# Optimization experiments

Hardware: AMD Instinct MI355X
Metric: run time of the kernel (lower is better)

## Reference

```python
import jax, jax.numpy as jnp
import numpy as np

DIM = 1024
H = 16
DQK = 64   # head_qk_dim = dim*expand_k / num_heads
DV = 64    # head_v_dim
DIN = 4    # dim_inner (fast-weight rows)
CHUNK = 16
BASE_LR = 1e-3
KS = 4     # short conv kernel size
LN_EPS = 1e-5


def short_conv(x, w):
    """Causal depthwise conv1d (kernel KS) + identity residual.
    x: [b, l, c], w: [c, KS] (tap j multiplies x[t - (KS-1) + j])."""
    b, l, c = x.shape
    xp = jnp.pad(x, ((0, 0), (KS - 1, 0), (0, 0)))
    y = x  # residual: y = conv(x) + x
    for j in range(KS):
        y = y + xp[:, j:j + l, :] * w[None, None, :, j]
    return y


def setup_inputs() -> dict:
    key = jax.random.key(0)
    ks = jax.random.split(key, 16)
    b, l = 4, 2048
    key_dim, value_dim = H * DQK, H * DV
    inp = {
        "hidden_states": jax.random.normal(ks[0], (b, l, DIM), jnp.float32),
        "Wq": jax.random.normal(ks[1], (key_dim, DIM), jnp.float32) / np.sqrt(DIM),
        "Wk": jax.random.normal(ks[2], (key_dim, DIM), jnp.float32) / np.sqrt(DIM),
        "Wv": jax.random.normal(ks[3], (value_dim, DIM), jnp.float32) / np.sqrt(DIM),
        "Wlr": jax.random.normal(ks[4], (2 * H, DIM), jnp.float32) / np.sqrt(DIM),
        "Wo": jax.random.normal(ks[5], (DIM, value_dim), jnp.float32) / np.sqrt(value_dim),
        "Wg": jax.random.normal(ks[6], (DIM, value_dim), jnp.float32) / np.sqrt(value_dim),
        "conv_q": jax.random.normal(ks[7], (key_dim, KS), jnp.float32) / np.sqrt(KS),
        "conv_k": jax.random.normal(ks[8], (key_dim, KS), jnp.float32) / np.sqrt(KS),
        "conv_v": jax.random.normal(ks[9], (value_dim, KS), jnp.float32) / np.sqrt(KS),
        "W_in_init": jax.random.normal(ks[10], (1, DIN, H, DQK), jnp.float32) / np.sqrt(DQK),
        "W_out_init": jax.random.normal(ks[11], (1, DIN, H, DV), jnp.float32) / np.sqrt(DIN),
        "ln_gamma": jnp.ones((DV,), jnp.float32),
        "ln_beta": jnp.zeros((DV,), jnp.float32),
    }
    return inp


def reference(hidden_states, Wq, Wk, Wv, Wlr, Wo, Wg,
              conv_q, conv_k, conv_v, W_in_init, W_out_init, ln_gamma, ln_beta):
    b, l, _ = hidden_states.shape
    scale = 1.0 / np.sqrt(DQK)

    q = short_conv(hidden_states @ Wq.T, conv_q).reshape(b, l, H, DQK)
    k = short_conv(hidden_states @ Wk.T, conv_k).reshape(b, l, H, DQK)
    v = short_conv(hidden_states @ Wv.T, conv_v).reshape(b, l, H, DV)

    lr = jax.nn.softplus(hidden_states @ Wlr.T + BASE_LR).reshape(b, l, H, 2)

    nC = l // CHUNK
    # [nC, b, CHUNK, H, d] for scan over chunks
    qc = q.reshape(b, nC, CHUNK, H, DQK).transpose(1, 0, 2, 3, 4)
    kc = k.reshape(b, nC, CHUNK, H, DQK).transpose(1, 0, 2, 3, 4)
    vc = v.reshape(b, nC, CHUNK, H, DV).transpose(1, 0, 2, 3, 4)
    lrc = lr.reshape(b, nC, CHUNK, H, 2).transpose(1, 0, 2, 3, 4)

    W_in0 = jnp.broadcast_to(W_in_init, (b, DIN, H, DQK))
    W_out0 = jnp.broadcast_to(W_out_init, (b, DIN, H, DV))

    # causal mask: query t (abs pos DIN+t) sees keys j <= DIN+t
    mask = jnp.arange(DIN + CHUNK)[None, :] <= (jnp.arange(CHUNK)[:, None] + DIN)

    def step(carry, xs):
        W_in, W_out = carry
        qch, kch, vch, lrch = xs  # [b, CHUNK, H, d]
        Kf = jnp.concatenate([W_in, kch], axis=1)   # [b, DIN+CHUNK, H, DQK]
        Vf = jnp.concatenate([W_out, vch], axis=1)  # [b, DIN+CHUNK, H, DV]
        s = jnp.einsum('bthd,bshd->bhts', qch, Kf) * scale
        s = jnp.where(mask[None, None], s, -jnp.inf)
        o = jnp.einsum('bhts,bshd->bthd', jax.nn.softmax(s, axis=-1), Vf)

        # fast_kk update rule (non-causal attention, queries = W_in rows)
        g1 = jnp.einsum('bnhd,bchd->bhnc', W_in, kch) * scale
        Grad_out = -jnp.einsum('bhnc,bchd->bnhd', jax.nn.softmax(g1, -1), vch)
        g2 = jnp.einsum('bnhd,bchd->bhnc', W_in, kch * 0.5) * scale
        Grad_in = -jnp.einsum('bhnc,bchd->bnhd', jax.nn.softmax(g2, -1), kch)

        lr_mean = jnp.mean(lrch, axis=1, keepdims=True)  # [b,1,H,2]
        W_in_new = W_in - lr_mean[..., 0:1] * Grad_in
        W_out_new = W_out - lr_mean[..., 1:2] * Grad_out
        return (W_in_new, W_out_new), o

    _, os = jax.lax.scan(step, (W_in0, W_out0), (qc, kc, vc, lrc))
    o = os.transpose(1, 0, 2, 3, 4).reshape(b, l, H, DV)

    # LayerNorm over head_v_dim
    mu = o.mean(-1, keepdims=True)
    var = o.var(-1, keepdims=True)
    o = (o - mu) / jnp.sqrt(var + LN_EPS) * ln_gamma + ln_beta
    o = o.reshape(b, l, H * DV)

    gate = hidden_states @ Wg.T
    return (o * gate) @ Wo.T
```

## Files before the change

kernel.cpp:

```cpp
#include <hip/hip_runtime.h>
#include <hip/hip_bf16.h>
#include <math.h>

#define BATCH 4
#define SEQ   2048
#define DIM   1024
#define NH    16
#define DQK   64
#define DV    64
#define DIN   4
#define CHUNK 16
#define NC    128
#define KS    4
#define TOK   (BATCH*SEQ)
#define SCALE 0.125f
#define BASE_LR 1e-3f
#define LN_EPS 1e-5f
#define K3    3072

typedef float f32x4 __attribute__((ext_vector_type(4)));
typedef short s16x8 __attribute__((ext_vector_type(8)));

__device__ __forceinline__ unsigned short f2bf(float f) {
    unsigned u = __float_as_uint(f);
    u += 0x7fffu + ((u >> 16) & 1u);
    return (unsigned short)(u >> 16);
}
__device__ __forceinline__ float bf2f(unsigned short h) {
    return __uint_as_float(((unsigned)h) << 16);
}

__device__ __forceinline__ void gload_lds16(const void* g, void* l) {
    __builtin_amdgcn_global_load_lds(
        (const __attribute__((address_space(1))) void*)g,
        (__attribute__((address_space(3))) void*)l, 16, 0, 0);
}

__global__ __launch_bounds__(256) void split_bf16_kernel(
    const float* __restrict__ X, unsigned short* __restrict__ Y,
    int rows, int wmode)
{
    const int idx = blockIdx.x * 256 + threadIdx.x;
    if (idx >= rows * (DIM / 4)) return;
    const int r  = idx >> 8;
    const int c4 = (idx & 255) << 2;

    float4 x = *(const float4*)(X + (size_t)r * DIM + c4);
    ushort4 hv, lv;
    hv.x = f2bf(x.x); lv.x = f2bf(x.x - bf2f(hv.x));
    hv.y = f2bf(x.y); lv.y = f2bf(x.y - bf2f(hv.y));
    hv.z = f2bf(x.z); lv.z = f2bf(x.z - bf2f(hv.z));
    hv.w = f2bf(x.w); lv.w = f2bf(x.w - bf2f(hv.w));

    const size_t rb = (size_t)r * K3;
    *(ushort4*)(Y + rb + c4)        = hv;
    *(ushort4*)(Y + rb + 1024 + c4) = wmode ? lv : hv;
    *(ushort4*)(Y + rb + 2048 + c4) = wmode ? hv : lv;
}

__global__ __launch_bounds__(256) void gemm_mfma_qkvg(
    const unsigned short* __restrict__ A, const unsigned short* __restrict__ B,
    float* __restrict__ Cq, float* __restrict__ Ck,
    float* __restrict__ Cv, float* __restrict__ Cg)
{
    __shared__ __align__(16) unsigned short sA[128 * 64];
    __shared__ __align__(16) unsigned short sB[128 * 64];

    const int tid  = threadIdx.x;
    const int lane = tid & 63;
    const int wav  = tid >> 6;

    const int nbx = gridDim.x;
    const int nwg = nbx * gridDim.y;
    int flat = blockIdx.x + blockIdx.y * nbx;
    const int per = nwg >> 3;
    flat = (flat & 7) * per + (flat >> 3);
    const int m0 = (flat / nbx) * 128;
    const int n0 = (flat % nbx) * 128;

    const int wm = (wav >> 1) * 64;
    const int wn = (wav & 1) * 64;

    f32x4 acc[4][4] = {};

    const int fbase = wav * 64 + lane;
    const int lrow  = lane & 15;
    const int g     = lane >> 4;

    for (int kt = 0; kt < K3; kt += 64) {
        __syncthreads();
#pragma unroll
        for (int i = 0; i < 4; ++i) {
            const int f  = fbase + i * 256;
            const int r  = f >> 3;
            const int c  = (f & 7) ^ (r & 7);
            const size_t go = (size_t)r * K3 + kt + c * 8;
            char* lb = (char*)sA + (wav * 64 + i * 256) * 16;
            gload_lds16(A + (size_t)m0 * K3 + go, lb);
        }
#pragma unroll
        for (int i = 0; i < 4; ++i) {
            const int f  = fbase + i * 256;
            const int r  = f >> 3;
            const int c  = (f & 7) ^ (r & 7);
            const size_t go = (size_t)r * K3 + kt + c * 8;
            char* lb = (char*)sB + (wav * 64 + i * 256) * 16;
            gload_lds16(B + (size_t)n0 * K3 + go, lb);
        }
        __syncthreads();

#pragma unroll
        for (int ks = 0; ks < 2; ++ks) {
            const int cbase = ks * 4 + g;
            s16x8 af[4], bfr[4];
#pragma unroll
            for (int mi = 0; mi < 4; ++mi) {
                const int r  = wm + mi * 16 + lrow;
                const int cs = cbase ^ (r & 7);
                af[mi] = *(const s16x8*)((const char*)sA + r * 128 + cs * 16);
            }
#pragma unroll
            for (int ni = 0; ni < 4; ++ni) {
                const int r  = wn + ni * 16 + lrow;
                const int cs = cbase ^ (r & 7);
                bfr[ni] = *(const s16x8*)((const char*)sB + r * 128 + cs * 16);
            }
#pragma unroll
            for (int mi = 0; mi < 4; ++mi)
#pragma unroll
                for (int ni = 0; ni < 4; ++ni)
                    acc[mi][ni] = __builtin_amdgcn_mfma_f32_16x16x32_bf16(
                        af[mi], bfr[ni], acc[mi][ni], 0, 0, 0);
        }
    }

    const int nblk = n0 >> 10;
    float* __restrict__ Co = (nblk == 0) ? Cq : (nblk == 1) ? Ck
                           : (nblk == 2) ? Cv : Cg;
    const int nc0 = (n0 & 1023) + wn;
    const int lcol = lane & 15;
    const int lq   = lane >> 4;
#pragma unroll
    for (int mi = 0; mi < 4; ++mi)
#pragma unroll
        for (int ni = 0; ni < 4; ++ni)
#pragma unroll
            for (int r = 0; r < 4; ++r) {
                const int m = m0 + wm + mi * 16 + lq * 4 + r;
                const int n = nc0 + ni * 16 + lcol;
                Co[(size_t)m * DIM + n] = acc[mi][ni][r];
            }
}

__global__ __launch_bounds__(256) void gemm_mfma_bt(
    const unsigned short* __restrict__ A, const unsigned short* __restrict__ B,
    float* __restrict__ C, int M, int N)
{
    __shared__ __align__(16) unsigned short sA[128 * 64];
    __shared__ __align__(16) unsigned short sB[128 * 64];

    const int tid  = threadIdx.x;
    const int lane = tid & 63;
    const int wav  = tid >> 6;

    const int nbx = gridDim.x;
    const int nwg = nbx * gridDim.y;
    int flat = blockIdx.x + blockIdx.y * nbx;
    const int per = nwg >> 3;
    flat = (flat & 7) * per + (flat >> 3);
    const int m0 = (flat / nbx) * 128;
    const int n0 = (flat % nbx) * 128;

    const int wm = (wav >> 1) * 64;
    const int wn = (wav & 1) * 64;

    f32x4 acc[4][4] = {};

    const int fbase = wav * 64 + lane;
    const int lrow  = lane & 15;
    const int g     = lane >> 4;

    for (int kt = 0; kt < K3; kt += 64) {
        __syncthreads();
#pragma unroll
        for (int i = 0; i < 4; ++i) {
            const int f  = fbase + i * 256;
            const int r  = f >> 3;
            const int c  = (f & 7) ^ (r & 7);
            const size_t go = (size_t)r * K3 + kt + c * 8;
            char* lb = (char*)sA + (wav * 64 + i * 256) * 16;
            gload_lds16(A + (size_t)m0 * K3 + go, lb);
        }
#pragma unroll
        for (int i = 0; i < 4; ++i) {
            const int f  = fbase + i * 256;
            const int r  = f >> 3;
            const int c  = (f & 7) ^ (r & 7);
            const size_t go = (size_t)r * K3 + kt + c * 8;
            char* lb = (char*)sB + (wav * 64 + i * 256) * 16;
            gload_lds16(B + (size_t)n0 * K3 + go, lb);
        }
        __syncthreads();

#pragma unroll
        for (int ks = 0; ks < 2; ++ks) {
            const int cbase = ks * 4 + g;
            s16x8 af[4], bfr[4];
#pragma unroll
            for (int mi = 0; mi < 4; ++mi) {
                const int r  = wm + mi * 16 + lrow;
                const int cs = cbase ^ (r & 7);
                af[mi] = *(const s16x8*)((const char*)sA + r * 128 + cs * 16);
            }
#pragma unroll
            for (int ni = 0; ni < 4; ++ni) {
                const int r  = wn + ni * 16 + lrow;
                const int cs = cbase ^ (r & 7);
                bfr[ni] = *(const s16x8*)((const char*)sB + r * 128 + cs * 16);
            }
#pragma unroll
            for (int mi = 0; mi < 4; ++mi)
#pragma unroll
                for (int ni = 0; ni < 4; ++ni)
                    acc[mi][ni] = __builtin_amdgcn_mfma_f32_16x16x32_bf16(
                        af[mi], bfr[ni], acc[mi][ni], 0, 0, 0);
        }
    }

    const int lcol = lane & 15;
    const int lq   = lane >> 4;
#pragma unroll
    for (int mi = 0; mi < 4; ++mi)
#pragma unroll
        for (int ni = 0; ni < 4; ++ni)
#pragma unroll
            for (int r = 0; r < 4; ++r) {
                const int m = m0 + wm + mi * 16 + lq * 4 + r;
                const int n = n0 + wn + ni * 16 + lcol;
                C[(size_t)m * N + n] = acc[mi][ni][r];
            }
}

#define GBM 128
#define GBN 128
#define GBK 8

__global__ __launch_bounds__(256) void gemm_nt_f32(
    const float* __restrict__ A, const float* __restrict__ B,
    float* __restrict__ C, int M, int N, int K)
{
    __shared__ float As[GBK][GBM + 4];
    __shared__ float Bs[GBK][GBN + 4];

    const int tid = threadIdx.x;
    const int m0 = blockIdx.y * GBM;
    const int n0 = blockIdx.x * GBN;
    const int la_m = tid >> 1;
    const int la_k = (tid & 1) << 2;
    const int tm = tid >> 4;
    const int tn = tid & 15;

    float acc[8][8] = {};

    const float* Arow = A + (size_t)(m0 + la_m) * K + la_k;
    const float* Brow = B + (size_t)(n0 + la_m) * K + la_k;
    const bool bvalid = (n0 + la_m) < N;

    for (int k0 = 0; k0 < K; k0 += GBK) {
        float4 av = *(const float4*)(Arow + k0);
        float4 bv = make_float4(0.f, 0.f, 0.f, 0.f);
        if (bvalid) bv = *(const float4*)(Brow + k0);

        __syncthreads();
        As[la_k + 0][la_m] = av.x; As[la_k + 1][la_m] = av.y;
        As[la_k + 2][la_m] = av.z; As[la_k + 3][la_m] = av.w;
        Bs[la_k + 0][la_m] = bv.x; Bs[la_k + 1][la_m] = bv.y;
        Bs[la_k + 2][la_m] = bv.z; Bs[la_k + 3][la_m] = bv.w;
        __syncthreads();

#pragma unroll
        for (int k = 0; k < GBK; ++k) {
            float4 a0 = *(const float4*)&As[k][tm * 8];
            float4 a1 = *(const float4*)&As[k][tm * 8 + 4];
            float4 b0 = *(const float4*)&Bs[k][tn * 8];
            float4 b1 = *(const float4*)&Bs[k][tn * 8 + 4];
            float a[8] = {a0.x, a0.y, a0.z, a0.w, a1.x, a1.y, a1.z, a1.w};
            float b[8] = {b0.x, b0.y, b0.z, b0.w, b1.x, b1.y, b1.z, b1.w};
#pragma unroll
            for (int i = 0; i < 8; ++i)
#pragma unroll
                for (int j = 0; j < 8; ++j)
                    acc[i][j] += a[i] * b[j];
        }
    }

#pragma unroll
    for (int i = 0; i < 8; ++i) {
        const int m = m0 + tm * 8 + i;
#pragma unroll
        for (int j = 0; j < 8; ++j) {
            const int n = n0 + tn * 8 + j;
            if (n < N) C[(size_t)m * N + n] = acc[i][j];
        }
    }
}

__global__ __launch_bounds__(256) void conv_res_kernel(
    const float* __restrict__ x, const float* __restrict__ w,
    float* __restrict__ y)
{
    const int tid = blockIdx.x * blockDim.x + threadIdx.x;
    if (tid >= TOK * 256) return;
    const int c4  = (tid & 255) << 2;
    const int row = tid >> 8;
    const int t   = row & (SEQ - 1);

    const float* xp = x + (size_t)row * DIM + c4;
    float4 acc = *(const float4*)xp;
    float4 w0 = *(const float4*)(w + (c4 + 0) * 4);
    float4 w1 = *(const float4*)(w + (c4 + 1) * 4);
    float4 w2 = *(const float4*)(w + (c4 + 2) * 4);
    float4 w3 = *(const float4*)(w + (c4 + 3) * 4);

#pragma unroll
    for (int j = 0; j < 4; ++j) {
        const int tt = t - 3 + j;
        if (tt >= 0) {
            float4 xv = *(const float4*)(xp + (j - 3) * DIM);
            acc.x += xv.x * ((&w0.x)[j]);
            acc.y += xv.y * ((&w1.x)[j]);
            acc.z += xv.z * ((&w2.x)[j]);
            acc.w += xv.w * ((&w3.x)[j]);
        }
    }
    *(float4*)(y + (size_t)row * DIM + c4) = acc;
}

__global__ __launch_bounds__(256) void lrmean_kernel(
    const float* __restrict__ lrpre, float* __restrict__ lrm)
{
    const int idx = blockIdx.x * blockDim.x + threadIdx.x;
    if (idx >= BATCH * NC * NH * 2) return;
    const int j = idx & 1;
    const int h = (idx >> 1) & 15;
    const int c = (idx >> 5) & 127;
    const int b = idx >> 12;

    float s = 0.f;
#pragma unroll
    for (int i = 0; i < CHUNK; ++i) {
        float x = lrpre[((size_t)b * SEQ + c * CHUNK + i) * 32 + h * 2 + j] + BASE_LR;
        s += fmaxf(x, 0.f) + log1pf(expf(-fabsf(x)));
    }
    lrm[idx] = s * (1.f / CHUNK);
}

__global__ __launch_bounds__(64) void state_scan_kernel(
    const float* __restrict__ kconv, const float* __restrict__ vconv,
    const float* __restrict__ lrm,
    const float* __restrict__ win_init, const float* __restrict__ wout_init,
    float* __restrict__ wst_in, float* __restrict__ wst_out)
{
    const int bh = blockIdx.x;
    const int b = bh >> 4, h = bh & 15;
    const int d = threadIdx.x;

    __shared__ __align__(16) float sW[DIN][68];
    __shared__ __align__(16) float sK[CHUNK][68];
    __shared__ __align__(16) float sP1[DIN][16];
    __shared__ __align__(16) float sP2[DIN][16];
    __shared__ float sLR[NC * 2];

    float win[DIN], wout[DIN];
#pragma unroll
    for (int n = 0; n < DIN; ++n) {
        win[n]  = win_init [(n * NH + h) * DQK + d];
        wout[n] = wout_init[(n * NH + h) * DV  + d];
    }
#pragma unroll
    for (int i = 0; i < 4; ++i) {
        const int idx = d * 4 + i;
        const int c = idx >> 1, j = idx & 1;
        sLR[idx] = lrm[(((size_t)b * NC + c) * NH + h) * 2 + j];
    }

    const int gn = d >> 4;
    const int gc = d & 15;

    float ka[CHUNK], va[CHUNK], kb[CHUNK], vb[CHUNK];

    const size_t base00 = (size_t)b * SEQ * DIM + h * 64 + d;
#pragma unroll
    for (int i = 0; i < CHUNK; ++i) {
        ka[i] = kconv[base00 + (size_t)i * DIM];
        va[i] = vconv[base00 + (size_t)i * DIM];
    }
    asm volatile("s_waitcnt lgkmcnt(0)" ::: "memory");

#define SCAN_STEP(c, KC, VC, KN, VN)                                           \
    {                                                                          \
        if ((c) + 1 < NC) {                                                    \
            const size_t basen = base00 + (size_t)(((c) + 1) * CHUNK) * DIM;   \
            _Pragma("unroll")                                                  \
            for (int i = 0; i < CHUNK; ++i) {                                  \
                KN[i] = kconv[basen + (size_t)i * DIM];                        \
                VN[i] = vconv[basen + (size_t)i * DIM];                        \
            }                                                                  \
        }                                                                      \
        const size_t wofs = (((size_t)bh * NC + (c)) * DIN) * 64 + d;          \
        _Pragma("unroll")                                                      \
        for (int n = 0; n < DIN; ++n) {                                        \
            wst_in [wofs + n * 64] = win[n];                                   \
            wst_out[wofs + n * 64] = wout[n];                                  \
        }                                                                      \
        _Pragma("unroll")                                                      \
        for (int i = 0; i < CHUNK; ++i) sK[i][d] = KC[i];                      \
        _Pragma("unroll")                                                      \
        for (int n = 0; n < DIN; ++n) sW[n][d] = win[n];                       \
        asm volatile("s_waitcnt lgkmcnt(0)" ::: "memory");                     \
        float dot = 0.f;                                                       \
        _Pragma("unroll")                                                      \
        for (int q = 0; q < 16; ++q) {                                         \
            float4 wv = *(const float4*)&sW[gn][q * 4];                        \
            float4 xv = *(const float4*)&sK[gc][q * 4];                        \
            dot += wv.x * xv.x; dot += wv.y * xv.y;                            \
            dot += wv.z * xv.z; dot += wv.w * xv.w;                            \
        }                                                                      \
        float g1 = dot * SCALE;                                                \
        float g2 = dot * (0.5f * SCALE);                                       \
        float m1 = g1, m2 = g2;                                                \
        _Pragma("unroll")                                                      \
        for (int mk = 8; mk >= 1; mk >>= 1) {                                  \
            m1 = fmaxf(m1, __shfl_xor(m1, mk, 16));                            \
            m2 = fmaxf(m2, __shfl_xor(m2, mk, 16));                            \
        }                                                                      \
        float e1 = expf(g1 - m1), e2 = expf(g2 - m2);                          \
        float s1 = e1, s2 = e2;                                                \
        _Pragma("unroll")                                                      \
        for (int mk = 8; mk >= 1; mk >>= 1) {                                  \
            s1 += __shfl_xor(s1, mk, 16);                                      \
            s2 += __shfl_xor(s2, mk, 16);                                      \
        }                                                                      \
        sP1[gn][gc] = e1 / s1;                                                 \
        sP2[gn][gc] = e2 / s2;                                                 \
        asm volatile("s_waitcnt lgkmcnt(0)" ::: "memory");                     \
        const float lr0 = sLR[(c) * 2 + 0];                                    \
        const float lr1 = sLR[(c) * 2 + 1];                                    \
        _Pragma("unroll")                                                      \
        for (int n = 0; n < DIN; ++n) {                                        \
            float aI = 0.f, aO = 0.f;                                          \
            _Pragma("unroll")                                                  \
            for (int q = 0; q < 4; ++q) {                                      \
                float4 p2 = *(const float4*)&sP2[n][q * 4];                    \
                float4 p1 = *(const float4*)&sP1[n][q * 4];                    \
                aI += p2.x * KC[q * 4 + 0]; aI += p2.y * KC[q * 4 + 1];        \
                aI += p2.z * KC[q * 4 + 2]; aI += p2.w * KC[q * 4 + 3];        \
                aO += p1.x * VC[q * 4 + 0]; aO += p1.y * VC[q * 4 + 1];        \
                aO += p1.z * VC[q * 4 + 2]; aO += p1.w * VC[q * 4 + 3];        \
            }                                                                  \
            win[n]  += lr0 * aI;                                               \
            wout[n] += lr1 * aO;                                               \
        }                                                                      \
        asm volatile("s_waitcnt lgkmcnt(0)" ::: "memory");                     \
    }

    for (int c = 0; c < NC; c += 2) {
        SCAN_STEP(c,     ka, va, kb, vb);
        SCAN_STEP(c + 1, kb, vb, ka, va);
    }
#undef SCAN_STEP
}

__global__ __launch_bounds__(64) void attn_kernel(
    const float* __restrict__ qconv, const float* __restrict__ kconv,
    const float* __restrict__ vconv,
    const float* __restrict__ wst_in, const float* __restrict__ wst_out,
    const float* __restrict__ gate,
    const float* __restrict__ gamma, const float* __restrict__ beta,
    float* __restrict__ og)
{
    const int blk = blockIdx.x;
    const int c  = blk & (NC - 1);
    const int bh = blk >> 7;
    const int h = bh & 15, b = bh >> 4;
    const int d = threadIdx.x;

    __shared__ float sQ[CHUNK][65];
    __shared__ float sKf[DIN + CHUNK][65];
    __shared__ float sS[CHUNK][21];
    __shared__ float sO[CHUNK][65];
    __shared__ float sMu[CHUNK], sRs[CHUNK];

    float vf[DIN + CHUNK];

    const size_t wofs = (size_t)blk * (DIN * 64) + d;
#pragma unroll
    for (int n = 0; n < DIN; ++n) {
        sKf[n][d] = wst_in [wofs + n * 64];
        vf[n]     = wst_out[wofs + n * 64];
    }
    const size_t base = ((size_t)b * SEQ + c * CHUNK) * DIM + h * 64 + d;
#pragma unroll
    for (int i = 0; i < CHUNK; ++i) {
        sQ[i][d]        = qconv[base + (size_t)i * DIM];
        sKf[DIN + i][d] = kconv[base + (size_t)i * DIM];
        vf[DIN + i]     = vconv[base + (size_t)i * DIM];
    }
    __syncthreads();

#pragma unroll
    for (int r = 0; r < 5; ++r) {
        const int p = d + 64 * r;
        const int t = p / 20, j = p % 20;
        float dot = 0.f;
#pragma unroll
        for (int dd = 0; dd < 64; ++dd) dot += sQ[t][dd] * sKf[j][dd];
        float s = dot * SCALE;
        if (j >= DIN && (j - DIN) > t) s = -3.0e38f;
        sS[t][j] = s;
    }
    __syncthreads();

    if (d < CHUNK) {
        float m = -3.0e38f;
#pragma unroll
        for (int j = 0; j < DIN + CHUNK; ++j) m = fmaxf(m, sS[d][j]);
        float e[DIN + CHUNK];
        float sum = 0.f;
#pragma unroll
        for (int j = 0; j < DIN + CHUNK; ++j) { e[j] = expf(sS[d][j] - m); sum += e[j]; }
        const float inv = 1.f / sum;
#pragma unroll
        for (int j = 0; j < DIN + CHUNK; ++j) sS[d][j] = e[j] * inv;
    }
    __syncthreads();

#pragma unroll
    for (int t = 0; t < CHUNK; ++t) {
        float o = 0.f;
#pragma unroll
        for (int j = 0; j < DIN + CHUNK; ++j) o += sS[t][j] * vf[j];
        sO[t][d] = o;
    }
    __syncthreads();

    if (d < CHUNK) {
        float su = 0.f, sq = 0.f;
#pragma unroll
        for (int dd = 0; dd < 64; ++dd) { float x = sO[d][dd]; su += x; sq += x * x; }
        float mu = su * (1.f / 64.f);
        float var = sq * (1.f / 64.f) - mu * mu;
        sMu[d] = mu;
        sRs[d] = rsqrtf(var + LN_EPS);
    }
    __syncthreads();

    const float gm = gamma[d], bt = beta[d];
#pragma unroll
    for (int t = 0; t < CHUNK; ++t) {
        float val = (sO[t][d] - sMu[t]) * sRs[t] * gm + bt;
        float gval = gate[base + (size_t)t * DIM];
        og[base + (size_t)t * DIM] = val * gval;
    }
}

extern "C" void kernel_launch(void* const* d_in, const int* in_sizes, int n_in,
                              void* d_out, int out_size, void* d_ws, size_t ws_size,
                              hipStream_t stream)
{
    const float* hid   = (const float*)d_in[0];
    const float* Wq    = (const float*)d_in[1];
    const float* Wk    = (const float*)d_in[2];
    const float* Wv    = (const float*)d_in[3];
    const float* Wlr   = (const float*)d_in[4];
    const float* Wo    = (const float*)d_in[5];
    const float* Wg    = (const float*)d_in[6];
    const float* cq    = (const float*)d_in[7];
    const float* ck    = (const float*)d_in[8];
    const float* cv    = (const float*)d_in[9];
    const float* wini  = (const float*)d_in[10];
    const float* wouti = (const float*)d_in[11];
    const float* lng   = (const float*)d_in[12];
    const float* lnb   = (const float*)d_in[13];
    float* out = (float*)d_out;

    float* ws = (float*)d_ws;
    const size_t DSZ = (size_t)TOK * DIM;
    float* qraw  = ws;
    float* kraw  = qraw + DSZ;
    float* vraw  = kraw + DSZ;
    float* gatb  = vraw + DSZ;
    float* lrpre = gatb + DSZ;
    float* lrm   = lrpre + (size_t)TOK * 32;
    float* wsti  = lrm   + BATCH * NC * NH * 2;
    float* wsto  = wsti  + (size_t)BATCH * NH * NC * DIN * 64;
    unsigned short* Abuf = (unsigned short*)(wsto + (size_t)BATCH * NH * NC * DIN * 64);
    unsigned short* Bbuf = Abuf + (size_t)TOK * K3;
    float* spar = (float*)Bbuf;

    float* qv = spar;
    float* kv = qraw;
    float* vv = kraw;

    const dim3 blk256(256);
    const dim3 fused_grid(32, 64);
    const dim3 out_grid(8, 64);
    const dim3 gemm_grid_lr(1, TOK / GBM);
    const int conv_blocks = (TOK * 256 + 255) / 256;

    split_bf16_kernel<<<TOK, blk256, 0, stream>>>(hid, Abuf, TOK, 0);
    split_bf16_kernel<<<1024, blk256, 0, stream>>>(Wq, Bbuf,                       1024, 1);
    split_bf16_kernel<<<1024, blk256, 0, stream>>>(Wk, Bbuf + (size_t)1024 * K3,   1024, 1);
    split_bf16_kernel<<<1024, blk256, 0, stream>>>(Wv, Bbuf + (size_t)2048 * K3,   1024, 1);
    split_bf16_kernel<<<1024, blk256, 0, stream>>>(Wg, Bbuf + (size_t)3072 * K3,   1024, 1);

    gemm_mfma_qkvg<<<fused_grid, blk256, 0, stream>>>(Abuf, Bbuf, qraw, kraw, vraw, gatb);

    conv_res_kernel<<<conv_blocks, blk256, 0, stream>>>(qraw, cq, spar);
    conv_res_kernel<<<conv_blocks, blk256, 0, stream>>>(kraw, ck, qraw);
    conv_res_kernel<<<conv_blocks, blk256, 0, stream>>>(vraw, cv, kraw);

    gemm_nt_f32<<<gemm_grid_lr, blk256, 0, stream>>>(hid, Wlr, lrpre, TOK, 32, DIM);
    lrmean_kernel<<<(BATCH * NC * NH * 2 + 255) / 256, blk256, 0, stream>>>(lrpre, lrm);

    state_scan_kernel<<<BATCH * NH, 64, 0, stream>>>(kv, vv, lrm, wini, wouti, wsti, wsto);
    attn_kernel<<<BATCH * NH * NC, 64, 0, stream>>>(qv, kv, vv, wsti, wsto,
                                                    gatb, lng, lnb, qv);

    split_bf16_kernel<<<TOK, blk256, 0, stream>>>(qv, Abuf, TOK, 0);
    split_bf16_kernel<<<1024, blk256, 0, stream>>>(Wo, Bbuf, 1024, 1);
    gemm_mfma_bt<<<out_grid, blk256, 0, stream>>>(Abuf, Bbuf, out, TOK, DIM);
}
```

Measured before the change: 982.5 us.

## Split state scan into two waves for W_in and W_out updates

The sequential state-scan kernel now runs 128 threads per (batch, head). One wave updates W_in from k and the other updates W_out from v, which halves per-thread register arrays and global loads. Wave 0 computes the attention logits once and derives the half-scale softmax by taking sqrt of exp(g1 - max), removing a second exp and max reduction. It also uses double-buffered probability tiles and splits dot-product accumulators for ILP, at the cost of a block barrier per chunk and a serial dependency on wave 0.

Result: faster. 917.8 us (-6.6%).

```diff
diff --git a/kernel.cpp b/kernel.cpp
--- a/kernel.cpp
+++ b/kernel.cpp
@@ -355,118 +355,120 @@
     lrm[idx] = s * (1.f / CHUNK);
 }
 
-__global__ __launch_bounds__(64) void state_scan_kernel(
+__global__ __launch_bounds__(128) void state_scan_kernel(
     const float* __restrict__ kconv, const float* __restrict__ vconv,
     const float* __restrict__ lrm,
     const float* __restrict__ win_init, const float* __restrict__ wout_init,
     float* __restrict__ wst_in, float* __restrict__ wst_out)
 {
-    const int bh = blockIdx.x;
-    const int b = bh >> 4, h = bh & 15;
-    const int d = threadIdx.x;
+    const int bh  = blockIdx.x;
+    const int b   = bh >> 4, h = bh & 15;
+    const int tid = threadIdx.x;
+    const int wv  = tid >> 6;
+    const int d   = tid & 63;
 
     __shared__ __align__(16) float sW[DIN][68];
     __shared__ __align__(16) float sK[CHUNK][68];
-    __shared__ __align__(16) float sP1[DIN][16];
-    __shared__ __align__(16) float sP2[DIN][16];
+    __shared__ __align__(16) float sP1[2][DIN][16];
+    __shared__ __align__(16) float sP2[2][DIN][16];
     __shared__ float sLR[NC * 2];
 
-    float win[DIN], wout[DIN];
-#pragma unroll
-    for (int n = 0; n < DIN; ++n) {
-        win[n]  = win_init [(n * NH + h) * DQK + d];
-        wout[n] = wout_init[(n * NH + h) * DV  + d];
-    }
-#pragma unroll
-    for (int i = 0; i < 4; ++i) {
-        const int idx = d * 4 + i;
-        const int c = idx >> 1, j = idx & 1;
-        sLR[idx] = lrm[(((size_t)b * NC + c) * NH + h) * 2 + j];
-    }
+    const float* __restrict__ xin  = wv ? vconv     : kconv;
+    const float* __restrict__ wini = wv ? wout_init : win_init;
+    float*       __restrict__ wst  = wv ? wst_out   : wst_in;
+
+    float W[DIN];
+#pragma unroll
+    for (int n = 0; n < DIN; ++n) W[n] = wini[(n * NH + h) * 64 + d];
+
+    sLR[tid * 2 + 0] = lrm[(((size_t)b * NC + tid) * NH + h) * 2 + 0];
+    sLR[tid * 2 + 1] = lrm[(((size_t)b * NC + tid) * NH + h) * 2 + 1];
 
     const int gn = d >> 4;
     const int gc = d & 15;
 
-    float ka[CHUNK], va[CHUNK], kb[CHUNK], vb[CHUNK];
-
+    float xa[CHUNK], xb[CHUNK];
     const size_t base00 = (size_t)b * SEQ * DIM + h * 64 + d;
 #pragma unroll
-    for (int i = 0; i < CHUNK; ++i) {
-        ka[i] = kconv[base00 + (size_t)i * DIM];
-        va[i] = vconv[base00 + (size_t)i * DIM];
-    }
+    for (int i = 0; i < CHUNK; ++i) xa[i] = xin[base00 + (size_t)i * DIM];
     asm volatile("s_waitcnt lgkmcnt(0)" ::: "memory");
 
-#define SCAN_STEP(c, KC, VC, KN, VN)                                           \
+#define SCAN_STEP(c, XA, XB)                                                   \
     {                                                                          \
+        const int pb = (c) & 1;                                                \
         if ((c) + 1 < NC) {                                                    \
             const size_t basen = base00 + (size_t)(((c) + 1) * CHUNK) * DIM;   \
             _Pragma("unroll")                                                  \
-            for (int i = 0; i < CHUNK; ++i) {                                  \
-                KN[i] = kconv[basen + (size_t)i * DIM];                        \
-                VN[i] = vconv[basen + (size_t)i * DIM];                        \
-            }                                                                  \
+            for (int i = 0; i < CHUNK; ++i)                                    \
+                XB[i] = xin[basen + (size_t)i * DIM];                          \
         }                                                                      \
         const size_t wofs = (((size_t)bh * NC + (c)) * DIN) * 64 + d;          \
         _Pragma("unroll")                                                      \
-        for (int n = 0; n < DIN; ++n) {                                        \
-            wst_in [wofs + n * 64] = win[n];                                   \
-            wst_out[wofs + n * 64] = wout[n];                                  \
+        for (int n = 0; n < DIN; ++n) wst[wofs + n * 64] = W[n];               \
+        if (wv == 0) {                                                         \
+            _Pragma("unroll")                                                  \
+            for (int i = 0; i < CHUNK; ++i) sK[i][d] = XA[i];                  \
+            _Pragma("unroll")                                                  \
+            for (int n = 0; n < DIN; ++n) sW[n][d] = W[n];                     \
+            asm volatile("s_waitcnt lgkmcnt(0)" ::: "memory");                 \
+            float p0 = 0.f, p1 = 0.f, p2 = 0.f, p3 = 0.f;                      \
+            _Pragma("unroll")                                                  \
+            for (int q = 0; q < 4; ++q) {                                      \
+                const int o = q * 16;                                          \
+                float4 w0 = *(const float4*)&sW[gn][o + 0];                    \
+                float4 k0 = *(const float4*)&sK[gc][o + 0];                    \
+                float4 w1 = *(const float4*)&sW[gn][o + 4];                    \
+                float4 k1 = *(const float4*)&sK[gc][o + 4];                    \
+                float4 w2 = *(const float4*)&sW[gn][o + 8];                    \
+                float4 k2 = *(const float4*)&sK[gc][o + 8];                    \
+                float4 w3 = *(const float4*)&sW[gn][o + 12];                   \
+                float4 k3 = *(const float4*)&sK[gc][o + 12];                   \
+                p0 += w0.x*k0.x; p0 += w0.y*k0.y; p0 += w0.z*k0.z; p0 += w0.w*k0.w; \
+                p1 += w1.x*k1.x; p1 += w1.y*k1.y; p1 += w1.z*k1.z; p1 += w1.w*k1.w; \
+                p2 += w2.x*k2.x; p2 += w2.y*k2.y; p2 += w2.z*k2.z; p2 += w2.w*k2.w; \
+                p3 += w3.x*k3.x; p3 += w3.y*k3.y; p3 += w3.z*k3.z; p3 += w3.w*k3.w; \
+            }                                                                  \
+            const float g1 = ((p0 + p1) + (p2 + p3)) * SCALE;                  \
+            float m = g1;                                                      \
+            _Pragma("unroll")                                                  \
+            for (int mk = 8; mk >= 1; mk >>= 1)                                \
+                m = fmaxf(m, __shfl_xor(m, mk, 16));                           \
+            const float e1 = expf(g1 - m);                                     \
+            const float rr = sqrtf(e1);                 \
+            float s1 = e1, s2 = rr;                                            \
+            _Pragma("unroll")                                                  \
+            for (int mk = 8; mk >= 1; mk >>= 1) {                              \
+                s1 += __shfl_xor(s1, mk, 16);                                  \
+                s2 += __shfl_xor(s2, mk, 16);                                  \
+            }                                                                  \
+            sP1[pb][gn][gc] = e1 / s1;                                         \
+            sP2[pb][gn][gc] = rr / s2;                                         \
+            asm volatile("s_waitcnt lgkmcnt(0)" ::: "memory");                 \
         }                                                                      \
-        _Pragma("unroll")                                                      \
-        for (int i = 0; i < CHUNK; ++i) sK[i][d] = KC[i];                      \
-        _Pragma("unroll")                                                      \
-        for (int n = 0; n < DIN; ++n) sW[n][d] = win[n];                       \
-        asm volatile("s_waitcnt lgkmcnt(0)" ::: "memory");                     \
-        float dot = 0.f;                                                       \
-        _Pragma("unroll")                                                      \
-        for (int q = 0; q < 16; ++q) {                                         \
-            float4 wv = *(const float4*)&sW[gn][q * 4];                        \
-            float4 xv = *(const float4*)&sK[gc][q * 4];                        \
-            dot += wv.x * xv.x; dot += wv.y * xv.y;                            \
-            dot += wv.z * xv.z; dot += wv.w * xv.w;                            \
-        }                                                                      \
-        float g1 = dot * SCALE;                                                \
-        float g2 = dot * (0.5f * SCALE);                                       \
-        float m1 = g1, m2 = g2;                                                \
-        _Pragma("unroll")                                                      \
-        for (int mk = 8; mk >= 1; mk >>= 1) {                                  \
-            m1 = fmaxf(m1, __shfl_xor(m1, mk, 16));                            \
-            m2 = fmaxf(m2, __shfl_xor(m2, mk, 16));                            \
-        }                                                                      \
-        float e1 = expf(g1 - m1), e2 = expf(g2 - m2);                          \
-        float s1 = e1, s2 = e2;                                                \
-        _Pragma("unroll")                                                      \
-        for (int mk = 8; mk >= 1; mk >>= 1) {                                  \
-            s1 += __shfl_xor(s1, mk, 16);                                      \
-            s2 += __shfl_xor(s2, mk, 16);                                      \
-        }                                                                      \
-        sP1[gn][gc] = e1 / s1;                                                 \
-        sP2[gn][gc] = e2 / s2;                                                 \
-        asm volatile("s_waitcnt lgkmcnt(0)" ::: "memory");                     \
-        const float lr0 = sLR[(c) * 2 + 0];                                    \
-        const float lr1 = sLR[(c) * 2 + 1];                                    \
+        __builtin_amdgcn_s_barrier();                                          \
+        const float lr = sLR[(c) * 2 + wv];                                    \
+        const float (*P)[16] = wv ? sP1[pb] : sP2[pb];                         \
         _Pragma("unroll")                                                      \
         for (int n = 0; n < DIN; ++n) {                                        \
-            float aI = 0.f, aO = 0.f;                                          \
-            _Pragma("unroll")                                                  \
-            for (int q = 0; q < 4; ++q) {                                      \
-                float4 p2 = *(const float4*)&sP2[n][q * 4];                    \
-                float4 p1 = *(const float4*)&sP1[n][q * 4];                    \
-                aI += p2.x * KC[q * 4 + 0]; aI += p2.y * KC[q * 4 + 1];        \
-                aI += p2.z * KC[q * 4 + 2]; aI += p2.w * KC[q * 4 + 3];        \
-                aO += p1.x * VC[q * 4 + 0]; aO += p1.y * VC[q * 4 + 1];        \
-                aO += p1.z * VC[q * 4 + 2]; aO += p1.w * VC[q * 4 + 3];        \
-            }                                                                  \
-            win[n]  += lr0 * aI;                                               \
-            wout[n] += lr1 * aO;                                               \
+            float4 q0 = *(const float4*)&P[n][0];                              \
+            float4 q1 = *(const float4*)&P[n][4];                              \
+            float4 q2 = *(const float4*)&P[n][8];                              \
+            float4 q3 = *(const float4*)&P[n][12];                             \
+            float t0 = q0.x*XA[0];  t0 += q0.y*XA[1];                          \
+            t0 += q0.z*XA[2];       t0 += q0.w*XA[3];                          \
+            float t1 = q1.x*XA[4];  t1 += q1.y*XA[5];                          \
+            t1 += q1.z*XA[6];       t1 += q1.w*XA[7];                          \
+            float t2 = q2.x*XA[8];  t2 += q2.y*XA[9];                          \
+            t2 += q2.z*XA[10];      t2 += q2.w*XA[11];                         \
+            float t3 = q3.x*XA[12]; t3 += q3.y*XA[13];                         \
+            t3 += q3.z*XA[14];      t3 += q3.w*XA[15];                         \
+            W[n] += lr * ((t0 + t1) + (t2 + t3));                              \
         }                                                                      \
-        asm volatile("s_waitcnt lgkmcnt(0)" ::: "memory");                     \
     }
 
     for (int c = 0; c < NC; c += 2) {
-        SCAN_STEP(c,     ka, va, kb, vb);
-        SCAN_STEP(c + 1, kb, vb, ka, va);
+        SCAN_STEP(c,     xa, xb);
+        SCAN_STEP(c + 1, xb, xa);
     }
 #undef SCAN_STEP
 }
@@ -623,7 +625,7 @@
     gemm_nt_f32<<<gemm_grid_lr, blk256, 0, stream>>>(hid, Wlr, lrpre, TOK, 32, DIM);
     lrmean_kernel<<<(BATCH * NC * NH * 2 + 255) / 256, blk256, 0, stream>>>(lrpre, lrm);
 
-    state_scan_kernel<<<BATCH * NH, 64, 0, stream>>>(kv, vv, lrm, wini, wouti, wsti, wsto);
+    state_scan_kernel<<<BATCH * NH, 128, 0, stream>>>(kv, vv, lrm, wini, wouti, wsti, wsto);
     attn_kernel<<<BATCH * NH * NC, 64, 0, stream>>>(qv, kv, vv, wsti, wsto,
                                                     gatb, lng, lnb, qv);
 
```
